# Kernel optimization log

Hardware: AMD Instinct MI355X
Metric: run time of the kernel (lower is better)

## Reference

```python
import jax, jax.numpy as jnp
import numpy as np

B, L, D, H = 4, 2048, 1024, 16
HD = D // H  # head_dim = 64


def setup_inputs() -> dict:
    key = jax.random.key(0)
    k1, k2, k3 = jax.random.split(key, 3)
    scale_in = 1.0 / np.sqrt(D)
    return {
        "x": jax.random.normal(k1, (B, L, D), dtype=jnp.float32),
        "Wqkv": jax.random.normal(k2, (D, 3 * D), dtype=jnp.float32) * scale_in,
        "Wout": jax.random.normal(k3, (D, D), dtype=jnp.float32) * scale_in,
        "bout": jnp.zeros((D,), dtype=jnp.float32),
    }


def reference(x, Wqkv, Wout, bout):
    b, l, d = x.shape
    # QKV projection (no bias): [B, L, 3D] -> [B, L, 3, H, HD]
    qkv = (x @ Wqkv).reshape(b, l, 3, H, HD)
    q, k, v = jnp.moveaxis(qkv, 2, 0)  # each [B, L, H, HD]
    # scaled scores [B, H, L, L]
    scores = jnp.einsum("blhd,bmhd->bhlm", q, k) / jnp.sqrt(jnp.float32(HD))
    causal_mask = jnp.triu(jnp.ones((l, l), dtype=bool), k=1)
    scores = jnp.where(causal_mask, -jnp.inf, scores)
    attn = jax.nn.softmax(scores, axis=-1)
    # dropout p=0.0 (eval-mode reference) -> identity
    out = jnp.einsum("bhlm,bmhd->blhd", attn, v).reshape(b, l, d)
    return out @ Wout + bout
```

## Files before the change

kernel.cpp:

```cpp
#include <hip/hip_runtime.h>

typedef unsigned short ushort_t;
using bf16x8 = __attribute__((ext_vector_type(8))) short;
using f32x4  = __attribute__((ext_vector_type(4))) float;
using f32x16 = __attribute__((ext_vector_type(16))) float;
using u32x4  = __attribute__((ext_vector_type(4))) unsigned int;

#define B_  4
#define L_  2048
#define D_  1024
#define H_  16
#define HD_ 64
#define N3_ 3072
#define M1_ (B_ * L_)

static __device__ __forceinline__ unsigned short f2bf(float f) {
    unsigned int u = __float_as_uint(f);
    unsigned int r = (u + 0x7fffu + ((u >> 16) & 1u)) >> 16;
    return (unsigned short)r;
}

static __device__ __forceinline__ unsigned int pkbf(float lo, float hi) {
    unsigned int r;
    asm("v_cvt_pk_bf16_f32 %0, %1, %2" : "=v"(r) : "v"(lo), "v"(hi));
    return r;
}

static __device__ __forceinline__ void plswap(unsigned int& a, unsigned int& b) {
    asm volatile("v_permlane32_swap_b32 %0, %1" : "+v"(a), "+v"(b));
}

static __device__ __forceinline__ void async16(const void* g, const void* l) {
    __builtin_amdgcn_global_load_lds(
        (const __attribute__((address_space(1))) void*)g,
        (__attribute__((address_space(3))) void*)l, 16, 0, 0);
}

__global__ void convert_x_kernel(const float4* __restrict__ src,
                                 ushort4* __restrict__ dst) {
    int i = blockIdx.x * blockDim.x + threadIdx.x;
    float4 v = src[i];
    ushort4 o;
    o.x = f2bf(v.x); o.y = f2bf(v.y); o.z = f2bf(v.z); o.w = f2bf(v.w);
    dst[i] = o;
}

__global__ void transpose_conv_kernel(const float* __restrict__ src,
                                      unsigned short* __restrict__ dst,
                                      int rows, int cols) {
    __shared__ float tile[32][33];
    int tx = threadIdx.x, ty = threadIdx.y;
    int c0 = blockIdx.x * 32, r0 = blockIdx.y * 32;
    #pragma unroll
    for (int j = 0; j < 32; j += 8)
        tile[ty + j][tx] = src[(size_t)(r0 + ty + j) * cols + c0 + tx];
    __syncthreads();
    #pragma unroll
    for (int j = 0; j < 32; j += 8)
        dst[(size_t)(c0 + ty + j) * rows + r0 + tx] = f2bf(tile[tx][ty + j]);
}

__global__ __launch_bounds__(512, 4) void gemm256_qkv_kernel(
    const unsigned short* __restrict__ A, const unsigned short* __restrict__ BT,
    unsigned short* __restrict__ qb, unsigned short* __restrict__ kb,
    unsigned short* __restrict__ vb) {
    constexpr int K = 1024, BK = 32, NT = K / BK;
    constexpr int NBX = N3_ / 128;
    constexpr int NWG = (M1_ / 256) * NBX;
    __shared__ __align__(16) unsigned short ldsA[2][256 * BK];
    __shared__ __align__(16) unsigned short ldsB[2][128 * BK];

    const int tid = threadIdx.x;
    const int w = tid >> 6, lane = tid & 63;
    const int wr = w >> 2, wc = w & 3;
    const int lg = lane >> 4, ll = lane & 15;

    const int bid = blockIdx.x;
    const int swz = (bid & 7) * (NWG / 8) + (bid >> 3);
    const int m0 = (swz / NBX) * 256, n0 = (swz % NBX) * 128;

    const int srow = tid >> 2;
    const int scol = (((tid & 3) ^ ((tid >> 3) & 3)) * 8);
    const int rxor = ((ll >> 1) & 3) * 8;

    f32x4 acc[8][2] = {};

    async16(&A[(size_t)(m0 + srow) * K + scol],        &ldsA[0][tid * 8]);
    async16(&A[(size_t)(m0 + 128 + srow) * K + scol],  &ldsA[0][4096 + tid * 8]);
    async16(&BT[(size_t)(n0 + srow) * K + scol],       &ldsB[0][tid * 8]);

    #pragma unroll 1
    for (int kt = 0; kt < NT; ++kt) {
        if (kt + 1 < NT) {
            const int buf = (kt + 1) & 1;
            const size_t koff = (size_t)(kt + 1) * BK + scol;
            async16(&A[(size_t)(m0 + srow) * K + koff],       &ldsA[buf][tid * 8]);
            async16(&A[(size_t)(m0 + 128 + srow) * K + koff], &ldsA[buf][4096 + tid * 8]);
            async16(&BT[(size_t)(n0 + srow) * K + koff],      &ldsB[buf][tid * 8]);
            asm volatile("s_waitcnt vmcnt(3)" ::: "memory");
        } else {
            asm volatile("s_waitcnt vmcnt(0)" ::: "memory");
        }
        __builtin_amdgcn_s_barrier();
        __builtin_amdgcn_sched_barrier(0);

        const unsigned short* Ab = &ldsA[kt & 1][0];
        const unsigned short* Bb = &ldsB[kt & 1][0];
        bf16x8 bf[2];
        #pragma unroll
        for (int j = 0; j < 2; ++j)
            bf[j] = *(const bf16x8*)&Bb[(wc * 32 + j * 16 + ll) * BK + (lg * 8 ^ rxor)];
        bf16x8 af[8];
        #pragma unroll
        for (int i = 0; i < 8; ++i)
            af[i] = *(const bf16x8*)&Ab[(wr * 128 + i * 16 + ll) * BK + (lg * 8 ^ rxor)];

        __builtin_amdgcn_s_setprio(1);
        #pragma unroll
        for (int i = 0; i < 8; ++i)
            #pragma unroll
            for (int j = 0; j < 2; ++j)
                acc[i][j] = __builtin_amdgcn_mfma_f32_16x16x32_bf16(
                    af[i], bf[j], acc[i][j], 0, 0, 0);
        __builtin_amdgcn_s_setprio(0);
        __builtin_amdgcn_s_barrier();
    }

    #pragma unroll
    for (int mi = 0; mi < 8; ++mi) {
        const int mb = m0 + wr * 128 + mi * 16 + lg * 4;
        #pragma unroll
        for (int ni = 0; ni < 2; ++ni) {
            const int n = n0 + wc * 32 + ni * 16 + ll;
            const int s = n >> 10, h = (n >> 6) & 15, hd = n & 63;
            if (s == 2) {
                const int b = mb >> 11, l = mb & 2047;
                const size_t base = (size_t)(b * H_ + h) * (L_ * HD_);
                ushort4 pk;
                pk.x = f2bf(acc[mi][ni][0]);
                pk.y = f2bf(acc[mi][ni][1]);
                pk.z = f2bf(acc[mi][ni][2]);
                pk.w = f2bf(acc[mi][ni][3]);
                *(ushort4*)&vb[base + (l >> 5) * 2048 + ((l >> 4) & 1) * 1024 +
                               ((l >> 3) & 1) * 512 + hd * 8 + (l & 7)] = pk;
            } else {
                #pragma unroll
                for (int r = 0; r < 4; ++r) {
                    const int m = mb + r;
                    const int b = m >> 11, l = m & 2047;
                    const size_t base = (size_t)(b * H_ + h) * (L_ * HD_);
                    const size_t o = base + (l >> 5) * 2048 + (hd >> 4) * 512 +
                                     ((hd >> 3) & 1) * 256 + (l & 31) * 8 + (hd & 7);
                    unsigned short bv = f2bf(acc[mi][ni][r]);
                    if (s == 0) qb[o] = bv; else kb[o] = bv;
                }
            }
        }
    }
}

__global__ __launch_bounds__(256) void gemm_bt_kernel(
    const unsigned short* __restrict__ A, const unsigned short* __restrict__ BT,
    float* __restrict__ outp, const float* __restrict__ bias) {
    constexpr int K = 1024;
    __shared__ unsigned short As[128 * 32];
    __shared__ unsigned short Bs[128 * 32];
    const int tid = threadIdx.x, w = tid >> 6, lane = tid & 63;
    const int m0 = blockIdx.y * 128, n0 = blockIdx.x * 128;
    const int wm = (w >> 1) * 64, wn = (w & 1) * 64;
    const int lg = lane >> 4, ll = lane & 15;
    const int scol = (((lane & 3) ^ ((lane >> 3) & 3)) * 8);
    const int rxor = ((ll >> 1) & 3) * 8;

    f32x4 acc[4][4] = {};

    for (int k0 = 0; k0 < K; k0 += 32) {
        #pragma unroll
        for (int j = 0; j < 2; ++j) {
            int row = w * 32 + j * 16 + (lane >> 2);
            async16(&A[(size_t)(m0 + row) * K + k0 + scol], &As[(w * 32 + j * 16) * 32]);
            async16(&BT[(size_t)(n0 + row) * K + k0 + scol], &Bs[(w * 32 + j * 16) * 32]);
        }
        __syncthreads();
        bf16x8 af[4], bfr[4];
        #pragma unroll
        for (int i = 0; i < 4; ++i) {
            af[i]  = *(const bf16x8*)&As[(wm + i * 16 + ll) * 32 + (lg * 8 ^ rxor)];
            bfr[i] = *(const bf16x8*)&Bs[(wn + i * 16 + ll) * 32 + (lg * 8 ^ rxor)];
        }
        #pragma unroll
        for (int mi = 0; mi < 4; ++mi)
            #pragma unroll
            for (int ni = 0; ni < 4; ++ni)
                acc[mi][ni] = __builtin_amdgcn_mfma_f32_16x16x32_bf16(
                    af[mi], bfr[ni], acc[mi][ni], 0, 0, 0);
        __syncthreads();
    }

    #pragma unroll
    for (int mi = 0; mi < 4; ++mi)
        #pragma unroll
        for (int ni = 0; ni < 4; ++ni)
            #pragma unroll
            for (int r = 0; r < 4; ++r) {
                int m = m0 + wm + mi * 16 + lg * 4 + r;
                int n = n0 + wn + ni * 16 + ll;
                outp[(size_t)m * D_ + n] = acc[mi][ni][r] + bias[n];
            }
}

__global__ __launch_bounds__(256) void attn_kernel(
    const unsigned short* __restrict__ qbuf, const unsigned short* __restrict__ kbuf,
    const unsigned short* __restrict__ vbuf, unsigned short* __restrict__ obuf) {
    __shared__ float Sden[4][32];

    const int tid = threadIdx.x;
    const int w = tid >> 6, lane = tid & 63;
    const int lq = lane & 31;
    const int hi = lane >> 5;

    const int bid = blockIdx.x;
    const int grp = bid >> 6;
    const int bh  = bid & 63;
    const int qt  = (15 - grp) * 4 + w;
    const int q0  = qt * 32;

    const unsigned short* Qf = qbuf + (size_t)bh * (L_ * HD_);
    const unsigned short* Kf = kbuf + (size_t)bh * (L_ * HD_);
    const unsigned short* Vf = vbuf + (size_t)bh * (L_ * HD_);

    bf16x8 qf[4];
    #pragma unroll
    for (int c = 0; c < 4; ++c)
        qf[c] = *(const bf16x8*)&Qf[qt * 2048 + c * 512 + hi * 256 + lq * 8];

    f32x16 oa0 = {}, oa1 = {};
    float sden = 0.f;

    const float C1 = 0.18033688011112042f;
    const float C2 = 7.2134752044448165f;

    const int ntiles = qt + 1;

    bf16x8 kf[4];
    #pragma unroll
    for (int c = 0; c < 4; ++c)
        kf[c] = *(const bf16x8*)&Kf[c * 512 + hi * 256 + lq * 8];

    for (int t = 0; t < ntiles; ++t) {
        bf16x8 v0f[2], v1f[2];
        #pragma unroll
        for (int c = 0; c < 2; ++c) {
            v0f[c] = *(const bf16x8*)&Vf[t * 2048 + c * 1024 + hi * 512 + lq * 8];
            v1f[c] = *(const bf16x8*)&Vf[t * 2048 + c * 1024 + hi * 512 + 256 + lq * 8];
        }
        bf16x8 nk[4];
        const bool more = (t + 1 < ntiles);
        if (more) {
            #pragma unroll
            for (int c = 0; c < 4; ++c)
                nk[c] = *(const bf16x8*)&Kf[(t + 1) * 2048 + c * 512 + hi * 256 + lq * 8];
        }

        f32x16 st = {};
        __builtin_amdgcn_s_setprio(1);
        #pragma unroll
        for (int c = 0; c < 4; ++c)
            st = __builtin_amdgcn_mfma_f32_32x32x16_bf16(kf[c], qf[c], st, 0, 0, 0);
        __builtin_amdgcn_s_setprio(0);

        float p[16];
        float rs = 0.f;
        const bool diag = (t == qt);
        #pragma unroll
        for (int r = 0; r < 16; ++r) {
            float pv = exp2f(fmaf(st[r], C1, -C2));
            if (diag) {
                int kv = (r & 3) + 8 * (r >> 2) + 4 * hi;
                if (kv > lq) pv = 0.f;
            }
            p[r] = pv;
            rs += pv;
        }
        rs += __shfl_xor(rs, 32);
        sden += rs;

        unsigned int a0 = pkbf(p[0],  p[1]),  a1 = pkbf(p[2],  p[3]);
        unsigned int b0 = pkbf(p[4],  p[5]),  b1 = pkbf(p[6],  p[7]);
        unsigned int c0 = pkbf(p[8],  p[9]),  c1 = pkbf(p[10], p[11]);
        unsigned int d0 = pkbf(p[12], p[13]), d1 = pkbf(p[14], p[15]);
        plswap(a0, b0);
        plswap(a1, b1);
        plswap(c0, d0);
        plswap(c1, d1);
        u32x4 t0 = {a0, a1, b0, b1};
        u32x4 t1 = {c0, c1, d0, d1};
        bf16x8 pa0 = __builtin_bit_cast(bf16x8, t0);
        bf16x8 pa1 = __builtin_bit_cast(bf16x8, t1);

        __builtin_amdgcn_s_setprio(1);
        oa0 = __builtin_amdgcn_mfma_f32_32x32x16_bf16(pa0, v0f[0], oa0, 0, 0, 0);
        oa1 = __builtin_amdgcn_mfma_f32_32x32x16_bf16(pa0, v1f[0], oa1, 0, 0, 0);
        oa0 = __builtin_amdgcn_mfma_f32_32x32x16_bf16(pa1, v0f[1], oa0, 0, 0, 0);
        oa1 = __builtin_amdgcn_mfma_f32_32x32x16_bf16(pa1, v1f[1], oa1, 0, 0, 0);
        __builtin_amdgcn_s_setprio(0);

        if (more) {
            #pragma unroll
            for (int c = 0; c < 4; ++c) kf[c] = nk[c];
        }
    }

    if (hi == 0) Sden[w][lq] = 1.0f / sden;
    __builtin_amdgcn_s_waitcnt(0);

    const int b = bh >> 4, h = bh & 15;
    #pragma unroll
    for (int r = 0; r < 16; ++r) {
        int q = (r & 3) + 8 * (r >> 2) + 4 * hi;
        float inv = Sden[w][q];
        float o0 = oa0[r] * inv;
        float o1 = oa1[r] * inv;
        size_t row = (size_t)(b * L_ + q0 + q) * D_ + h * HD_;
        obuf[row + lq]      = f2bf(o0);
        obuf[row + 32 + lq] = f2bf(o1);
    }
}

extern "C" void kernel_launch(void* const* d_in, const int* in_sizes, int n_in,
                              void* d_out, int out_size, void* d_ws, size_t ws_size,
                              hipStream_t stream) {
    const float* x    = (const float*)d_in[0];
    const float* Wqkv = (const float*)d_in[1];
    const float* Wout = (const float*)d_in[2];
    const float* bout = (const float*)d_in[3];
    float* out = (float*)d_out;

    char* ws = (char*)d_ws;
    size_t off = 0;
    unsigned short* xb     = (unsigned short*)(ws + off); off += (size_t)M1_ * D_ * 2;
    unsigned short* wqkvT  = (unsigned short*)(ws + off); off += (size_t)N3_ * D_ * 2;
    unsigned short* woutT  = (unsigned short*)(ws + off); off += (size_t)D_ * D_ * 2;
    unsigned short* qb     = (unsigned short*)(ws + off); off += (size_t)B_ * H_ * L_ * HD_ * 2;
    unsigned short* kb     = (unsigned short*)(ws + off); off += (size_t)B_ * H_ * L_ * HD_ * 2;
    unsigned short* vb     = (unsigned short*)(ws + off); off += (size_t)B_ * H_ * L_ * HD_ * 2;
    unsigned short* attnb  = (unsigned short*)(ws + off); off += (size_t)M1_ * D_ * 2;

    convert_x_kernel<<<(M1_ * D_ / 4) / 256, 256, 0, stream>>>(
        (const float4*)x, (ushort4*)xb);
    transpose_conv_kernel<<<dim3(N3_ / 32, D_ / 32), dim3(32, 8), 0, stream>>>(
        Wqkv, wqkvT, D_, N3_);
    transpose_conv_kernel<<<dim3(D_ / 32, D_ / 32), dim3(32, 8), 0, stream>>>(
        Wout, woutT, D_, D_);

    gemm256_qkv_kernel<<<dim3((M1_ / 256) * (N3_ / 128)), 512, 0, stream>>>(
        xb, wqkvT, qb, kb, vb);

    attn_kernel<<<dim3(16 * 64), 256, 0, stream>>>(qb, kb, vb, attnb);

    gemm_bt_kernel<<<dim3(D_ / 128, M1_ / 128), 256, 0, stream>>>(
        attnb, woutT, out, bout);
}
```

Baseline: 186.4 us.

## Deepen QKV GEMM pipeline to three stages with BK=64 and new LDS swizzle

The QKV projection GEMM now uses a K-tile of 64 instead of 32 and a triple-buffered LDS ring that prefetches two tiles ahead, with vmcnt waits adjusted to match. The LDS swizzle becomes an XOR over 8 slots, and the MFMA loop is split into four phases that interleave A-fragment loads with compute. The aim is to halve the number of barriers per K and hide global-load latency better. In exchange it uses much more LDS (about 144 KB), which lowers occupancy, reflected in launch bounds dropping from 4 to 2.

```diff
diff --git a/kernel.cpp b/kernel.cpp
--- a/kernel.cpp
+++ b/kernel.cpp
@@ -60,15 +60,15 @@
         dst[(size_t)(c0 + ty + j) * rows + r0 + tx] = f2bf(tile[tx][ty + j]);
 }
 
-__global__ __launch_bounds__(512, 4) void gemm256_qkv_kernel(
+__global__ __launch_bounds__(512, 2) void gemm256_qkv_kernel(
     const unsigned short* __restrict__ A, const unsigned short* __restrict__ BT,
     unsigned short* __restrict__ qb, unsigned short* __restrict__ kb,
     unsigned short* __restrict__ vb) {
-    constexpr int K = 1024, BK = 32, NT = K / BK;
+    constexpr int K = 1024, BK = 64, NT = K / BK;
     constexpr int NBX = N3_ / 128;
     constexpr int NWG = (M1_ / 256) * NBX;
-    __shared__ __align__(16) unsigned short ldsA[2][256 * BK];
-    __shared__ __align__(16) unsigned short ldsB[2][128 * BK];
+    __shared__ __align__(16) unsigned short ldsA[3][256 * BK];
+    __shared__ __align__(16) unsigned short ldsB[3][128 * BK];
 
     const int tid = threadIdx.x;
     const int w = tid >> 6, lane = tid & 63;
@@ -79,52 +79,80 @@
     const int swz = (bid & 7) * (NWG / 8) + (bid >> 3);
     const int m0 = (swz / NBX) * 256, n0 = (swz % NBX) * 128;
 
-    const int srow = tid >> 2;
-    const int scol = (((tid & 3) ^ ((tid >> 3) & 3)) * 8);
-    const int rxor = ((ll >> 1) & 3) * 8;
+    const int srow  = w * 8 + (lane >> 3);
+    const int gslot = (lane & 7) ^ (lane >> 3);
+    const int rsw   = ll & 7;
 
     f32x4 acc[8][2] = {};
 
-    async16(&A[(size_t)(m0 + srow) * K + scol],        &ldsA[0][tid * 8]);
-    async16(&A[(size_t)(m0 + 128 + srow) * K + scol],  &ldsA[0][4096 + tid * 8]);
-    async16(&BT[(size_t)(n0 + srow) * K + scol],       &ldsB[0][tid * 8]);
+    #define STAGE(kt_) do {                                                  \
+        const int b3_ = (kt_) % 3;                                           \
+        const size_t kbase_ = (size_t)(kt_) * BK + gslot * 8;                \
+        _Pragma("unroll")                                                    \
+        for (int rd = 0; rd < 4; ++rd)                                       \
+            async16(&A[(size_t)(m0 + rd * 64 + srow) * K + kbase_],          \
+                    &ldsA[b3_][rd * 4096 + w * 512 + lane * 8]);             \
+        _Pragma("unroll")                                                    \
+        for (int rd = 0; rd < 2; ++rd)                                       \
+            async16(&BT[(size_t)(n0 + rd * 64 + srow) * K + kbase_],         \
+                    &ldsB[b3_][rd * 4096 + w * 512 + lane * 8]);             \
+    } while (0)
+
+    STAGE(0);
+    STAGE(1);
 
     #pragma unroll 1
     for (int kt = 0; kt < NT; ++kt) {
-        if (kt + 1 < NT) {
-            const int buf = (kt + 1) & 1;
-            const size_t koff = (size_t)(kt + 1) * BK + scol;
-            async16(&A[(size_t)(m0 + srow) * K + koff],       &ldsA[buf][tid * 8]);
-            async16(&A[(size_t)(m0 + 128 + srow) * K + koff], &ldsA[buf][4096 + tid * 8]);
-            async16(&BT[(size_t)(n0 + srow) * K + koff],      &ldsB[buf][tid * 8]);
-            asm volatile("s_waitcnt vmcnt(3)" ::: "memory");
+        if (kt + 2 < NT) {
+            STAGE(kt + 2);
+            asm volatile("s_waitcnt vmcnt(12)" ::: "memory");
+        } else if (kt + 1 < NT) {
+            asm volatile("s_waitcnt vmcnt(6)" ::: "memory");
         } else {
             asm volatile("s_waitcnt vmcnt(0)" ::: "memory");
         }
         __builtin_amdgcn_s_barrier();
         __builtin_amdgcn_sched_barrier(0);
 
-        const unsigned short* Ab = &ldsA[kt & 1][0];
-        const unsigned short* Bb = &ldsB[kt & 1][0];
-        bf16x8 bf[2];
+        const int cb = kt % 3;
+        const unsigned short* Ab = &ldsA[cb][0];
+        const unsigned short* Bb = &ldsB[cb][0];
+
+        bf16x8 bfr[2][2];
         #pragma unroll
         for (int j = 0; j < 2; ++j)
-            bf[j] = *(const bf16x8*)&Bb[(wc * 32 + j * 16 + ll) * BK + (lg * 8 ^ rxor)];
-        bf16x8 af[8];
-        #pragma unroll
-        for (int i = 0; i < 8; ++i)
-            af[i] = *(const bf16x8*)&Ab[(wr * 128 + i * 16 + ll) * BK + (lg * 8 ^ rxor)];
-
-        __builtin_amdgcn_s_setprio(1);
-        #pragma unroll
-        for (int i = 0; i < 8; ++i)
-            #pragma unroll
-            for (int j = 0; j < 2; ++j)
-                acc[i][j] = __builtin_amdgcn_mfma_f32_16x16x32_bf16(
-                    af[i], bf[j], acc[i][j], 0, 0, 0);
-        __builtin_amdgcn_s_setprio(0);
+            #pragma unroll
+            for (int ks = 0; ks < 2; ++ks)
+                bfr[j][ks] = *(const bf16x8*)
+                    &Bb[(wc * 32 + j * 16 + ll) * BK + (((ks * 4 + lg) ^ rsw) * 8)];
+
+        #pragma unroll
+        for (int p = 0; p < 4; ++p) {
+            bf16x8 af[2][2];
+            #pragma unroll
+            for (int i = 0; i < 2; ++i)
+                #pragma unroll
+                for (int ks = 0; ks < 2; ++ks)
+                    af[i][ks] = *(const bf16x8*)
+                        &Ab[(wr * 128 + (p * 2 + i) * 16 + ll) * BK +
+                            (((ks * 4 + lg) ^ rsw) * 8)];
+            asm volatile("s_waitcnt lgkmcnt(0)" ::: "memory");
+            __builtin_amdgcn_sched_barrier(0);
+            __builtin_amdgcn_s_setprio(1);
+            #pragma unroll
+            for (int i = 0; i < 2; ++i)
+                #pragma unroll
+                for (int j = 0; j < 2; ++j)
+                    #pragma unroll
+                    for (int ks = 0; ks < 2; ++ks)
+                        acc[p * 2 + i][j] = __builtin_amdgcn_mfma_f32_16x16x32_bf16(
+                            af[i][ks], bfr[j][ks], acc[p * 2 + i][j], 0, 0, 0);
+            __builtin_amdgcn_s_setprio(0);
+            __builtin_amdgcn_sched_barrier(0);
+        }
         __builtin_amdgcn_s_barrier();
     }
+    #undef STAGE
 
     #pragma unroll
     for (int mi = 0; mi < 8; ++mi) {
```

Result: slower. 191.9 us (+2.9%).

## Triple-buffer the GEMM pipeline and reuse it for the output projection

Applied to the files above, without the earlier changes.

Turns the QKV GEMM into a template with a three-stage LDS pipeline that prefetches two k-tiles ahead, waiting on vmcnt(6) instead of the previous double buffering. The simple single-buffered 128x128 output-projection GEMM is replaced by the same 256x128, 512-thread pipelined kernel with a bias epilogue. This aims to hide global-load latency better in both GEMMs, at the cost of more LDS per block (72KB), which may lower occupancy. The out-projection grid also shrinks to 256 blocks, which may leave some CUs underused.

```diff
diff --git a/kernel.cpp b/kernel.cpp
--- a/kernel.cpp
+++ b/kernel.cpp
@@ -60,15 +60,17 @@
         dst[(size_t)(c0 + ty + j) * rows + r0 + tx] = f2bf(tile[tx][ty + j]);
 }
 
-__global__ __launch_bounds__(512, 4) void gemm256_qkv_kernel(
+template <int OUT_N, int EPI>
+__global__ __launch_bounds__(512, 4) void gemm256_kernel(
     const unsigned short* __restrict__ A, const unsigned short* __restrict__ BT,
     unsigned short* __restrict__ qb, unsigned short* __restrict__ kb,
-    unsigned short* __restrict__ vb) {
+    unsigned short* __restrict__ vb, float* __restrict__ outp,
+    const float* __restrict__ bias) {
     constexpr int K = 1024, BK = 32, NT = K / BK;
-    constexpr int NBX = N3_ / 128;
+    constexpr int NBX = OUT_N / 128;
     constexpr int NWG = (M1_ / 256) * NBX;
-    __shared__ __align__(16) unsigned short ldsA[2][256 * BK];
-    __shared__ __align__(16) unsigned short ldsB[2][128 * BK];
+    __shared__ __align__(16) unsigned short ldsA[3][256 * BK];
+    __shared__ __align__(16) unsigned short ldsB[3][128 * BK];
 
     const int tid = threadIdx.x;
     const int w = tid >> 6, lane = tid & 63;
@@ -85,18 +87,23 @@
 
     f32x4 acc[8][2] = {};
 
-    async16(&A[(size_t)(m0 + srow) * K + scol],        &ldsA[0][tid * 8]);
-    async16(&A[(size_t)(m0 + 128 + srow) * K + scol],  &ldsA[0][4096 + tid * 8]);
-    async16(&BT[(size_t)(n0 + srow) * K + scol],       &ldsB[0][tid * 8]);
+    #define STAGE(kt_) do {                                                  \
+        const int b3_ = (kt_) % 3;                                           \
+        const size_t koff_ = (size_t)(kt_) * BK + scol;                      \
+        async16(&A[(size_t)(m0 + srow) * K + koff_],       &ldsA[b3_][tid * 8]);        \
+        async16(&A[(size_t)(m0 + 128 + srow) * K + koff_], &ldsA[b3_][4096 + tid * 8]); \
+        async16(&BT[(size_t)(n0 + srow) * K + koff_],      &ldsB[b3_][tid * 8]);        \
+    } while (0)
+
+    STAGE(0);
+    STAGE(1);
 
     #pragma unroll 1
     for (int kt = 0; kt < NT; ++kt) {
-        if (kt + 1 < NT) {
-            const int buf = (kt + 1) & 1;
-            const size_t koff = (size_t)(kt + 1) * BK + scol;
-            async16(&A[(size_t)(m0 + srow) * K + koff],       &ldsA[buf][tid * 8]);
-            async16(&A[(size_t)(m0 + 128 + srow) * K + koff], &ldsA[buf][4096 + tid * 8]);
-            async16(&BT[(size_t)(n0 + srow) * K + koff],      &ldsB[buf][tid * 8]);
+        if (kt + 2 < NT) {
+            STAGE(kt + 2);
+            asm volatile("s_waitcnt vmcnt(6)" ::: "memory");
+        } else if (kt + 1 < NT) {
             asm volatile("s_waitcnt vmcnt(3)" ::: "memory");
         } else {
             asm volatile("s_waitcnt vmcnt(0)" ::: "memory");
@@ -104,12 +111,12 @@
         __builtin_amdgcn_s_barrier();
         __builtin_amdgcn_sched_barrier(0);
 
-        const unsigned short* Ab = &ldsA[kt & 1][0];
-        const unsigned short* Bb = &ldsB[kt & 1][0];
-        bf16x8 bf[2];
+        const unsigned short* Ab = &ldsA[kt % 3][0];
+        const unsigned short* Bb = &ldsB[kt % 3][0];
+        bf16x8 bfr[2];
         #pragma unroll
         for (int j = 0; j < 2; ++j)
-            bf[j] = *(const bf16x8*)&Bb[(wc * 32 + j * 16 + ll) * BK + (lg * 8 ^ rxor)];
+            bfr[j] = *(const bf16x8*)&Bb[(wc * 32 + j * 16 + ll) * BK + (lg * 8 ^ rxor)];
         bf16x8 af[8];
         #pragma unroll
         for (int i = 0; i < 8; ++i)
@@ -121,10 +128,11 @@
             #pragma unroll
             for (int j = 0; j < 2; ++j)
                 acc[i][j] = __builtin_amdgcn_mfma_f32_16x16x32_bf16(
-                    af[i], bf[j], acc[i][j], 0, 0, 0);
+                    af[i], bfr[j], acc[i][j], 0, 0, 0);
         __builtin_amdgcn_s_setprio(0);
         __builtin_amdgcn_s_barrier();
     }
+    #undef STAGE
 
     #pragma unroll
     for (int mi = 0; mi < 8; ++mi) {
@@ -132,81 +140,37 @@
         #pragma unroll
         for (int ni = 0; ni < 2; ++ni) {
             const int n = n0 + wc * 32 + ni * 16 + ll;
-            const int s = n >> 10, h = (n >> 6) & 15, hd = n & 63;
-            if (s == 2) {
-                const int b = mb >> 11, l = mb & 2047;
-                const size_t base = (size_t)(b * H_ + h) * (L_ * HD_);
-                ushort4 pk;
-                pk.x = f2bf(acc[mi][ni][0]);
-                pk.y = f2bf(acc[mi][ni][1]);
-                pk.z = f2bf(acc[mi][ni][2]);
-                pk.w = f2bf(acc[mi][ni][3]);
-                *(ushort4*)&vb[base + (l >> 5) * 2048 + ((l >> 4) & 1) * 1024 +
-                               ((l >> 3) & 1) * 512 + hd * 8 + (l & 7)] = pk;
+            if (EPI == 1) {
+                #pragma unroll
+                for (int r = 0; r < 4; ++r)
+                    outp[(size_t)(mb + r) * D_ + n] = acc[mi][ni][r] + bias[n];
             } else {
-                #pragma unroll
-                for (int r = 0; r < 4; ++r) {
-                    const int m = mb + r;
-                    const int b = m >> 11, l = m & 2047;
+                const int s = n >> 10, h = (n >> 6) & 15, hd = n & 63;
+                if (s == 2) {
+                    const int b = mb >> 11, l = mb & 2047;
                     const size_t base = (size_t)(b * H_ + h) * (L_ * HD_);
-                    const size_t o = base + (l >> 5) * 2048 + (hd >> 4) * 512 +
-                                     ((hd >> 3) & 1) * 256 + (l & 31) * 8 + (hd & 7);
-                    unsigned short bv = f2bf(acc[mi][ni][r]);
-                    if (s == 0) qb[o] = bv; else kb[o] = bv;
+                    ushort4 pk;
+                    pk.x = f2bf(acc[mi][ni][0]);
+                    pk.y = f2bf(acc[mi][ni][1]);
+                    pk.z = f2bf(acc[mi][ni][2]);
+                    pk.w = f2bf(acc[mi][ni][3]);
+                    *(ushort4*)&vb[base + (l >> 5) * 2048 + ((l >> 4) & 1) * 1024 +
+                                   ((l >> 3) & 1) * 512 + hd * 8 + (l & 7)] = pk;
+                } else {
+                    #pragma unroll
+                    for (int r = 0; r < 4; ++r) {
+                        const int m = mb + r;
+                        const int b = m >> 11, l = m & 2047;
+                        const size_t base = (size_t)(b * H_ + h) * (L_ * HD_);
+                        const size_t o = base + (l >> 5) * 2048 + (hd >> 4) * 512 +
+                                         ((hd >> 3) & 1) * 256 + (l & 31) * 8 + (hd & 7);
+                        unsigned short bv = f2bf(acc[mi][ni][r]);
+                        if (s == 0) qb[o] = bv; else kb[o] = bv;
+                    }
                 }
             }
         }
     }
-}
-
-__global__ __launch_bounds__(256) void gemm_bt_kernel(
-    const unsigned short* __restrict__ A, const unsigned short* __restrict__ BT,
-    float* __restrict__ outp, const float* __restrict__ bias) {
-    constexpr int K = 1024;
-    __shared__ unsigned short As[128 * 32];
-    __shared__ unsigned short Bs[128 * 32];
-    const int tid = threadIdx.x, w = tid >> 6, lane = tid & 63;
-    const int m0 = blockIdx.y * 128, n0 = blockIdx.x * 128;
-    const int wm = (w >> 1) * 64, wn = (w & 1) * 64;
-    const int lg = lane >> 4, ll = lane & 15;
-    const int scol = (((lane & 3) ^ ((lane >> 3) & 3)) * 8);
-    const int rxor = ((ll >> 1) & 3) * 8;
-
-    f32x4 acc[4][4] = {};
-
-    for (int k0 = 0; k0 < K; k0 += 32) {
-        #pragma unroll
-        for (int j = 0; j < 2; ++j) {
-            int row = w * 32 + j * 16 + (lane >> 2);
-            async16(&A[(size_t)(m0 + row) * K + k0 + scol], &As[(w * 32 + j * 16) * 32]);
-            async16(&BT[(size_t)(n0 + row) * K + k0 + scol], &Bs[(w * 32 + j * 16) * 32]);
-        }
-        __syncthreads();
-        bf16x8 af[4], bfr[4];
-        #pragma unroll
-        for (int i = 0; i < 4; ++i) {
-            af[i]  = *(const bf16x8*)&As[(wm + i * 16 + ll) * 32 + (lg * 8 ^ rxor)];
-            bfr[i] = *(const bf16x8*)&Bs[(wn + i * 16 + ll) * 32 + (lg * 8 ^ rxor)];
-        }
-        #pragma unroll
-        for (int mi = 0; mi < 4; ++mi)
-            #pragma unroll
-            for (int ni = 0; ni < 4; ++ni)
-                acc[mi][ni] = __builtin_amdgcn_mfma_f32_16x16x32_bf16(
-                    af[mi], bfr[ni], acc[mi][ni], 0, 0, 0);
-        __syncthreads();
-    }
-
-    #pragma unroll
-    for (int mi = 0; mi < 4; ++mi)
-        #pragma unroll
-        for (int ni = 0; ni < 4; ++ni)
-            #pragma unroll
-            for (int r = 0; r < 4; ++r) {
-                int m = m0 + wm + mi * 16 + lg * 4 + r;
-                int n = n0 + wn + ni * 16 + ll;
-                outp[(size_t)m * D_ + n] = acc[mi][ni][r] + bias[n];
-            }
 }
 
 __global__ __launch_bounds__(256) void attn_kernel(
@@ -353,11 +317,11 @@
     transpose_conv_kernel<<<dim3(D_ / 32, D_ / 32), dim3(32, 8), 0, stream>>>(
         Wout, woutT, D_, D_);
 
-    gemm256_qkv_kernel<<<dim3((M1_ / 256) * (N3_ / 128)), 512, 0, stream>>>(
-        xb, wqkvT, qb, kb, vb);
+    gemm256_kernel<N3_, 0><<<dim3((M1_ / 256) * (N3_ / 128)), 512, 0, stream>>>(
+        xb, wqkvT, qb, kb, vb, nullptr, nullptr);
 
     attn_kernel<<<dim3(16 * 64), 256, 0, stream>>>(qb, kb, vb, attnb);
 
-    gemm_bt_kernel<<<dim3(D_ / 128, M1_ / 128), 256, 0, stream>>>(
-        attnb, woutT, out, bout);
-}
+    gemm256_kernel<D_, 1><<<dim3((M1_ / 256) * (D_ / 128)), 512, 0, stream>>>(
+        attnb, woutT, nullptr, nullptr, nullptr, out, bout);
+}
```

Result: no change. 189.2 us (+1.5%).

## Triple-buffer QKV GEMM loads and share K/V tiles via LDS in attention

Applied to the files above, without the earlier changes.

The QKV GEMM moves from double to triple buffering of its LDS tiles, issuing loads two k-steps ahead with matching vmcnt waits so more global latency is hidden. The attention kernel stops having each wave load K and V fragments from global memory on its own. All four waves of a block now cooperatively async-copy each K/V tile into double-buffered LDS and read fragments from there, which cuts redundant global traffic. In exchange, waves with fewer causal tiles idle at barriers until the block's longest wave finishes, and the GEMM's larger LDS footprint may lower occupancy.

```diff
diff --git a/kernel.cpp b/kernel.cpp
--- a/kernel.cpp
+++ b/kernel.cpp
@@ -67,8 +67,8 @@
     constexpr int K = 1024, BK = 32, NT = K / BK;
     constexpr int NBX = N3_ / 128;
     constexpr int NWG = (M1_ / 256) * NBX;
-    __shared__ __align__(16) unsigned short ldsA[2][256 * BK];
-    __shared__ __align__(16) unsigned short ldsB[2][128 * BK];
+    __shared__ __align__(16) unsigned short ldsA[3][256 * BK];
+    __shared__ __align__(16) unsigned short ldsB[3][128 * BK];
 
     const int tid = threadIdx.x;
     const int w = tid >> 6, lane = tid & 63;
@@ -85,18 +85,23 @@
 
     f32x4 acc[8][2] = {};
 
-    async16(&A[(size_t)(m0 + srow) * K + scol],        &ldsA[0][tid * 8]);
-    async16(&A[(size_t)(m0 + 128 + srow) * K + scol],  &ldsA[0][4096 + tid * 8]);
-    async16(&BT[(size_t)(n0 + srow) * K + scol],       &ldsB[0][tid * 8]);
+    #define STAGE(kt_) do {                                                  \
+        const int b3_ = (kt_) % 3;                                           \
+        const size_t koff_ = (size_t)(kt_) * BK + scol;                      \
+        async16(&A[(size_t)(m0 + srow) * K + koff_],       &ldsA[b3_][tid * 8]);        \
+        async16(&A[(size_t)(m0 + 128 + srow) * K + koff_], &ldsA[b3_][4096 + tid * 8]); \
+        async16(&BT[(size_t)(n0 + srow) * K + koff_],      &ldsB[b3_][tid * 8]);        \
+    } while (0)
+
+    STAGE(0);
+    STAGE(1);
 
     #pragma unroll 1
     for (int kt = 0; kt < NT; ++kt) {
-        if (kt + 1 < NT) {
-            const int buf = (kt + 1) & 1;
-            const size_t koff = (size_t)(kt + 1) * BK + scol;
-            async16(&A[(size_t)(m0 + srow) * K + koff],       &ldsA[buf][tid * 8]);
-            async16(&A[(size_t)(m0 + 128 + srow) * K + koff], &ldsA[buf][4096 + tid * 8]);
-            async16(&BT[(size_t)(n0 + srow) * K + koff],      &ldsB[buf][tid * 8]);
+        if (kt + 2 < NT) {
+            STAGE(kt + 2);
+            asm volatile("s_waitcnt vmcnt(6)" ::: "memory");
+        } else if (kt + 1 < NT) {
             asm volatile("s_waitcnt vmcnt(3)" ::: "memory");
         } else {
             asm volatile("s_waitcnt vmcnt(0)" ::: "memory");
@@ -104,12 +109,12 @@
         __builtin_amdgcn_s_barrier();
         __builtin_amdgcn_sched_barrier(0);
 
-        const unsigned short* Ab = &ldsA[kt & 1][0];
-        const unsigned short* Bb = &ldsB[kt & 1][0];
-        bf16x8 bf[2];
+        const unsigned short* Ab = &ldsA[kt % 3][0];
+        const unsigned short* Bb = &ldsB[kt % 3][0];
+        bf16x8 bfr[2];
         #pragma unroll
         for (int j = 0; j < 2; ++j)
-            bf[j] = *(const bf16x8*)&Bb[(wc * 32 + j * 16 + ll) * BK + (lg * 8 ^ rxor)];
+            bfr[j] = *(const bf16x8*)&Bb[(wc * 32 + j * 16 + ll) * BK + (lg * 8 ^ rxor)];
         bf16x8 af[8];
         #pragma unroll
         for (int i = 0; i < 8; ++i)
@@ -121,10 +126,11 @@
             #pragma unroll
             for (int j = 0; j < 2; ++j)
                 acc[i][j] = __builtin_amdgcn_mfma_f32_16x16x32_bf16(
-                    af[i], bf[j], acc[i][j], 0, 0, 0);
+                    af[i], bfr[j], acc[i][j], 0, 0, 0);
         __builtin_amdgcn_s_setprio(0);
         __builtin_amdgcn_s_barrier();
     }
+    #undef STAGE
 
     #pragma unroll
     for (int mi = 0; mi < 8; ++mi) {
@@ -212,6 +218,8 @@
 __global__ __launch_bounds__(256) void attn_kernel(
     const unsigned short* __restrict__ qbuf, const unsigned short* __restrict__ kbuf,
     const unsigned short* __restrict__ vbuf, unsigned short* __restrict__ obuf) {
+    __shared__ __align__(16) unsigned short ldsK[2][2048];
+    __shared__ __align__(16) unsigned short ldsV[2][2048];
     __shared__ float Sden[4][32];
 
     const int tid = threadIdx.x;
@@ -224,6 +232,7 @@
     const int bh  = bid & 63;
     const int qt  = (15 - grp) * 4 + w;
     const int q0  = qt * 32;
+    const int ntmax = (15 - grp) * 4 + 4;
 
     const unsigned short* Qf = qbuf + (size_t)bh * (L_ * HD_);
     const unsigned short* Kf = kbuf + (size_t)bh * (L_ * HD_);
@@ -240,75 +249,75 @@
     const float C1 = 0.18033688011112042f;
     const float C2 = 7.2134752044448165f;
 
-    const int ntiles = qt + 1;
-
-    bf16x8 kf[4];
-    #pragma unroll
-    for (int c = 0; c < 4; ++c)
-        kf[c] = *(const bf16x8*)&Kf[c * 512 + hi * 256 + lq * 8];
-
-    for (int t = 0; t < ntiles; ++t) {
-        bf16x8 v0f[2], v1f[2];
-        #pragma unroll
-        for (int c = 0; c < 2; ++c) {
-            v0f[c] = *(const bf16x8*)&Vf[t * 2048 + c * 1024 + hi * 512 + lq * 8];
-            v1f[c] = *(const bf16x8*)&Vf[t * 2048 + c * 1024 + hi * 512 + 256 + lq * 8];
-        }
-        bf16x8 nk[4];
-        const bool more = (t + 1 < ntiles);
-        if (more) {
-            #pragma unroll
-            for (int c = 0; c < 4; ++c)
-                nk[c] = *(const bf16x8*)&Kf[(t + 1) * 2048 + c * 512 + hi * 256 + lq * 8];
-        }
-
-        f32x16 st = {};
-        __builtin_amdgcn_s_setprio(1);
-        #pragma unroll
-        for (int c = 0; c < 4; ++c)
-            st = __builtin_amdgcn_mfma_f32_32x32x16_bf16(kf[c], qf[c], st, 0, 0, 0);
-        __builtin_amdgcn_s_setprio(0);
-
-        float p[16];
-        float rs = 0.f;
-        const bool diag = (t == qt);
-        #pragma unroll
-        for (int r = 0; r < 16; ++r) {
-            float pv = exp2f(fmaf(st[r], C1, -C2));
-            if (diag) {
-                int kv = (r & 3) + 8 * (r >> 2) + 4 * hi;
-                if (kv > lq) pv = 0.f;
-            }
-            p[r] = pv;
-            rs += pv;
-        }
-        rs += __shfl_xor(rs, 32);
-        sden += rs;
-
-        unsigned int a0 = pkbf(p[0],  p[1]),  a1 = pkbf(p[2],  p[3]);
-        unsigned int b0 = pkbf(p[4],  p[5]),  b1 = pkbf(p[6],  p[7]);
-        unsigned int c0 = pkbf(p[8],  p[9]),  c1 = pkbf(p[10], p[11]);
-        unsigned int d0 = pkbf(p[12], p[13]), d1 = pkbf(p[14], p[15]);
-        plswap(a0, b0);
-        plswap(a1, b1);
-        plswap(c0, d0);
-        plswap(c1, d1);
-        u32x4 t0 = {a0, a1, b0, b1};
-        u32x4 t1 = {c0, c1, d0, d1};
-        bf16x8 pa0 = __builtin_bit_cast(bf16x8, t0);
-        bf16x8 pa1 = __builtin_bit_cast(bf16x8, t1);
-
-        __builtin_amdgcn_s_setprio(1);
-        oa0 = __builtin_amdgcn_mfma_f32_32x32x16_bf16(pa0, v0f[0], oa0, 0, 0, 0);
-        oa1 = __builtin_amdgcn_mfma_f32_32x32x16_bf16(pa0, v1f[0], oa1, 0, 0, 0);
-        oa0 = __builtin_amdgcn_mfma_f32_32x32x16_bf16(pa1, v0f[1], oa0, 0, 0, 0);
-        oa1 = __builtin_amdgcn_mfma_f32_32x32x16_bf16(pa1, v1f[1], oa1, 0, 0, 0);
-        __builtin_amdgcn_s_setprio(0);
-
-        if (more) {
-            #pragma unroll
-            for (int c = 0; c < 4; ++c) kf[c] = nk[c];
-        }
+    async16(&Kf[tid * 8], &ldsK[0][tid * 8]);
+    async16(&Vf[tid * 8], &ldsV[0][tid * 8]);
+
+    #pragma unroll 1
+    for (int t = 0; t < ntmax; ++t) {
+        if (t + 1 < ntmax) {
+            async16(&Kf[(size_t)(t + 1) * 2048 + tid * 8], &ldsK[(t + 1) & 1][tid * 8]);
+            async16(&Vf[(size_t)(t + 1) * 2048 + tid * 8], &ldsV[(t + 1) & 1][tid * 8]);
+            asm volatile("s_waitcnt vmcnt(2)" ::: "memory");
+        } else {
+            asm volatile("s_waitcnt vmcnt(0)" ::: "memory");
+        }
+        __builtin_amdgcn_s_barrier();
+        __builtin_amdgcn_sched_barrier(0);
+
+        if (t <= qt) {
+            const unsigned short* Kb = &ldsK[t & 1][0];
+            const unsigned short* Vb = &ldsV[t & 1][0];
+
+            f32x16 st = {};
+            __builtin_amdgcn_s_setprio(1);
+            #pragma unroll
+            for (int c = 0; c < 4; ++c) {
+                bf16x8 kf = *(const bf16x8*)&Kb[c * 512 + hi * 256 + lq * 8];
+                st = __builtin_amdgcn_mfma_f32_32x32x16_bf16(kf, qf[c], st, 0, 0, 0);
+            }
+            __builtin_amdgcn_s_setprio(0);
+
+            float p[16];
+            float rs = 0.f;
+            const bool diag = (t == qt);
+            #pragma unroll
+            for (int r = 0; r < 16; ++r) {
+                float pv = exp2f(fmaf(st[r], C1, -C2));
+                if (diag) {
+                    int kv = (r & 3) + 8 * (r >> 2) + 4 * hi;
+                    if (kv > lq) pv = 0.f;
+                }
+                p[r] = pv;
+                rs += pv;
+            }
+            rs += __shfl_xor(rs, 32);
+            sden += rs;
+
+            unsigned int a0 = pkbf(p[0],  p[1]),  a1 = pkbf(p[2],  p[3]);
+            unsigned int b0 = pkbf(p[4],  p[5]),  b1 = pkbf(p[6],  p[7]);
+            unsigned int c0 = pkbf(p[8],  p[9]),  c1 = pkbf(p[10], p[11]);
+            unsigned int d0 = pkbf(p[12], p[13]), d1 = pkbf(p[14], p[15]);
+            plswap(a0, b0);
+            plswap(a1, b1);
+            plswap(c0, d0);
+            plswap(c1, d1);
+            u32x4 t0 = {a0, a1, b0, b1};
+            u32x4 t1 = {c0, c1, d0, d1};
+            bf16x8 pa0 = __builtin_bit_cast(bf16x8, t0);
+            bf16x8 pa1 = __builtin_bit_cast(bf16x8, t1);
+
+            __builtin_amdgcn_s_setprio(1);
+            #pragma unroll
+            for (int c = 0; c < 2; ++c) {
+                bf16x8 v0f = *(const bf16x8*)&Vb[c * 1024 + hi * 512 + lq * 8];
+                bf16x8 v1f = *(const bf16x8*)&Vb[c * 1024 + hi * 512 + 256 + lq * 8];
+                bf16x8 pa = (c == 0) ? pa0 : pa1;
+                oa0 = __builtin_amdgcn_mfma_f32_32x32x16_bf16(pa, v0f, oa0, 0, 0, 0);
+                oa1 = __builtin_amdgcn_mfma_f32_32x32x16_bf16(pa, v1f, oa1, 0, 0, 0);
+            }
+            __builtin_amdgcn_s_setprio(0);
+        }
+        __builtin_amdgcn_s_barrier();
     }
 
     if (hi == 0) Sden[w][lq] = 1.0f / sden;
```

After: 199.1 us. +6.8%, slower.
